# Optimization experiments

Hardware: AMD Instinct MI355X
Metric: run time of the kernel (lower is better)

Reference implementation:

```python
import jax, jax.numpy as jnp
import numpy as np

C, K, D = 64, 512, 2048   # classes, shots per class, hidden_dim
N_ITER = 3                # n_routing_iter


def _squash(x):
    # x: (..., d); squash along last axis: x * ||x|| / (1 + ||x||^2)
    n2 = jnp.sum(x * x, axis=-1, keepdims=True)
    n = jnp.sqrt(n2)
    return x * (n / (1.0 + n2))


def setup_inputs() -> dict:
    key = jax.random.key(0)
    z_s = jax.random.normal(key, (C, K, D), dtype=jnp.float32)
    return {"z_s": z_s}


def reference(z_s):
    # z_s: (C, K, D). All C classes routed in parallel (vectorized over the
    # original Python loop over classes).
    z_sq = _squash(z_s)                       # (C, K, D)
    b = jnp.zeros(z_s.shape[:2], z_s.dtype)   # routing logits (C, K)
    c = jnp.zeros((z_s.shape[0], z_s.shape[2]), z_s.dtype)
    for _ in range(N_ITER):
        d = jax.nn.softmax(b, axis=-1)                      # (C, K)
        c = _squash(jnp.einsum('ck,ckd->cd', d, z_sq))      # (C, D)
        b = b + jnp.einsum('ckd,cd->ck', z_sq, c)           # (C, K)
    # returned representative is c from the LAST iteration (b update after is unused,
    # matching the torch loop where c_i from the final iter is appended)
    return c
```

## Files before the change

### kernel.cpp

```cpp
#include <hip/hip_runtime.h>
#include <math.h>

#define C_CLS   64
#define K_SHOTS 512
#define D_DIM   2048
#define BPC     16
#define ROWS_PER_BLOCK (K_SHOTS / BPC)
#define NWAVES  4
#define ROWS_PER_WAVE (ROWS_PER_BLOCK / NWAVES)
#define NBLK    (C_CLS * BPC)
#define NF4     8

__device__ __forceinline__ float wave_reduce_sum(float v) {
#pragma unroll
    for (int off = 32; off > 0; off >>= 1)
        v += __shfl_xor(v, off, 64);
    return v;
}

template <int PASS>
__global__ __launch_bounds__(256)
void route_pass(const float* __restrict__ z,
                float* __restrict__ scale,
                float* __restrict__ bvec,
                const float* __restrict__ c_prev,
                float* __restrict__ part_s,
                float* __restrict__ part_e)
{
    __shared__ float4 s_comb[NWAVES][D_DIM / 4];
    __shared__ float  e_comb[NWAVES];

    const int rawblk = blockIdx.x;
    const int blk  = (PASS == 1) ? (NBLK - 1 - rawblk) : rawblk;
    const int cls  = blk >> 4;
    const int bic  = blk & (BPC - 1);
    const int lane = threadIdx.x & 63;
    const int wid  = threadIdx.x >> 6;
    const int t    = threadIdx.x;

    float4 cp[NF4];
    if (PASS != 0) {
        const float4* cp4 = (const float4*)(c_prev + (size_t)cls * D_DIM);
#pragma unroll
        for (int i = 0; i < NF4; ++i) cp[i] = cp4[lane + i * 64];
    }

    float4 acc[NF4];
#pragma unroll
    for (int i = 0; i < NF4; ++i) acc[i] = make_float4(0.f, 0.f, 0.f, 0.f);
    float esum = 0.f;

    const int k0 = bic * ROWS_PER_BLOCK + wid * ROWS_PER_WAVE;
    const float4* __restrict__ zbase =
        (const float4*)(z + ((size_t)cls * K_SHOTS + k0) * D_DIM);

    const int r0    = (PASS == 1) ? (ROWS_PER_WAVE - 1) : 0;
    const int rstep = (PASS == 1) ? -1 : 1;

    float4 zcur[NF4];
#pragma unroll
    for (int i = 0; i < NF4; ++i) zcur[i] = zbase[(size_t)r0 * (D_DIM / 4) + lane + i * 64];

#pragma unroll
    for (int rr = 0; rr < ROWS_PER_WAVE; ++rr) {
        const int r = r0 + rr * rstep;
        float4 znext[NF4];
        if (rr + 1 < ROWS_PER_WAVE) {
            const float4* zn = zbase + (size_t)(r + rstep) * (D_DIM / 4);
#pragma unroll
            for (int i = 0; i < NF4; ++i) znext[i] = zn[lane + i * 64];
        }
        const int k = k0 + r;
        float w, sc;
        if (PASS == 0) {
            float n2 = 0.f;
#pragma unroll
            for (int i = 0; i < NF4; ++i)
                n2 += zcur[i].x * zcur[i].x + zcur[i].y * zcur[i].y
                    + zcur[i].z * zcur[i].z + zcur[i].w * zcur[i].w;
            n2 = wave_reduce_sum(n2);
            sc = sqrtf(n2) / (1.f + n2);
            if (lane == 0) scale[cls * K_SHOTS + k] = sc;
            w = 1.f;
        } else {
            float dot = 0.f;
#pragma unroll
            for (int i = 0; i < NF4; ++i)
                dot += zcur[i].x * cp[i].x + zcur[i].y * cp[i].y
                     + zcur[i].z * cp[i].z + zcur[i].w * cp[i].w;
            dot = wave_reduce_sum(dot);
            sc = scale[cls * K_SHOTS + k];
            float bnew = sc * dot;
            if (PASS == 2) bnew += bvec[cls * K_SHOTS + k];
            if (PASS == 1 && lane == 0) bvec[cls * K_SHOTS + k] = bnew;
            w = expf(bnew);
        }
        esum += w;
        const float wsc = w * sc;
#pragma unroll
        for (int i = 0; i < NF4; ++i) {
            acc[i].x += wsc * zcur[i].x;
            acc[i].y += wsc * zcur[i].y;
            acc[i].z += wsc * zcur[i].z;
            acc[i].w += wsc * zcur[i].w;
        }
        if (rr + 1 < ROWS_PER_WAVE) {
#pragma unroll
            for (int i = 0; i < NF4; ++i) zcur[i] = znext[i];
        }
    }

#pragma unroll
    for (int i = 0; i < NF4; ++i) s_comb[wid][lane + i * 64] = acc[i];
    if (lane == 0) e_comb[wid] = esum;
    __syncthreads();

    float4* ps = (float4*)(part_s + (size_t)blk * D_DIM);
#pragma unroll
    for (int j = 0; j < 2; ++j) {
        const int f = t + j * 256;
        const float4 a  = s_comb[0][f];
        const float4 b4 = s_comb[1][f];
        const float4 c4 = s_comb[2][f];
        const float4 d4 = s_comb[3][f];
        float4 s;
        s.x = (a.x + b4.x) + (c4.x + d4.x);
        s.y = (a.y + b4.y) + (c4.y + d4.y);
        s.z = (a.z + b4.z) + (c4.z + d4.z);
        s.w = (a.w + b4.w) + (c4.w + d4.w);
        ps[f] = s;
    }
    if (t == 0) part_e[blk] = (e_comb[0] + e_comb[1]) + (e_comb[2] + e_comb[3]);
}

__global__ __launch_bounds__(256)
void reduce_squash(const float* __restrict__ part_s,
                   const float* __restrict__ part_e,
                   float* __restrict__ c_out)
{
    __shared__ float wred[NWAVES];
    const int cls  = blockIdx.x;
    const int t    = threadIdx.x;
    const int lane = t & 63;
    const int wid  = t >> 6;

    float esum = 0.f;
#pragma unroll
    for (int p = 0; p < BPC; ++p) esum += part_e[cls * BPC + p];
    const float inv = 1.f / esum;

    float4 m[2];
    float n2p = 0.f;
#pragma unroll
    for (int j = 0; j < 2; ++j) {
        const int f = t + j * 256;
        float4 s = make_float4(0.f, 0.f, 0.f, 0.f);
        for (int p = 0; p < BPC; ++p) {
            const float4 v =
                ((const float4*)(part_s + (size_t)(cls * BPC + p) * D_DIM))[f];
            s.x += v.x; s.y += v.y; s.z += v.z; s.w += v.w;
        }
        m[j].x = s.x * inv; m[j].y = s.y * inv;
        m[j].z = s.z * inv; m[j].w = s.w * inv;
        n2p += m[j].x * m[j].x + m[j].y * m[j].y
             + m[j].z * m[j].z + m[j].w * m[j].w;
    }
    float n2 = wave_reduce_sum(n2p);
    if (lane == 0) wred[wid] = n2;
    __syncthreads();
    n2 = (wred[0] + wred[1]) + (wred[2] + wred[3]);
    const float fac = sqrtf(n2) / (1.f + n2);

    float4* co = (float4*)(c_out + (size_t)cls * D_DIM);
#pragma unroll
    for (int j = 0; j < 2; ++j) {
        const int f = t + j * 256;
        float4 o;
        o.x = m[j].x * fac; o.y = m[j].y * fac;
        o.z = m[j].z * fac; o.w = m[j].w * fac;
        co[f] = o;
    }
}

extern "C" void kernel_launch(void* const* d_in, const int* in_sizes, int n_in,
                              void* d_out, int out_size, void* d_ws, size_t ws_size,
                              hipStream_t stream)
{
    const float* z = (const float*)d_in[0];
    float* out = (float*)d_out;
    float* ws  = (float*)d_ws;

    float* scale  = ws;
    float* bvec   = scale + C_CLS * K_SHOTS;
    float* c_buf  = bvec + C_CLS * K_SHOTS;
    float* part_s = c_buf + (size_t)C_CLS * D_DIM;
    float* part_e = part_s + (size_t)NBLK * D_DIM;

    route_pass<0><<<NBLK, 256, 0, stream>>>(z, scale, bvec, nullptr, part_s, part_e);
    reduce_squash<<<C_CLS, 256, 0, stream>>>(part_s, part_e, c_buf);

    route_pass<1><<<NBLK, 256, 0, stream>>>(z, scale, bvec, c_buf, part_s, part_e);
    reduce_squash<<<C_CLS, 256, 0, stream>>>(part_s, part_e, c_buf);

    route_pass<2><<<NBLK, 256, 0, stream>>>(z, scale, bvec, c_buf, part_s, part_e);
    reduce_squash<<<C_CLS, 256, 0, stream>>>(part_s, part_e, out);
}
```

Baseline: 156.6 us.

## Store pre-squashed inputs as fp16 and stream them in later routing passes

The first pass reads fp32 z with nontemporal loads, computes the squash scale, and writes a pre-scaled fp16 copy of z_sq to workspace. The two later routing passes read this half-size copy and drop the per-row scale lookup. This cuts HBM traffic for the bandwidth-bound later passes and may let the fp16 copy stay in the last-level cache. In exchange it adds a 134 MB write, needs a large workspace, and loses precision from fp16 rounding of the inputs.

After: 151.6 us. 1.03x faster.

```diff
diff --git a/kernel.cpp b/kernel.cpp
--- a/kernel.cpp
+++ b/kernel.cpp
@@ -1,4 +1,5 @@
 #include <hip/hip_runtime.h>
+#include <hip/hip_fp16.h>
 #include <math.h>
 
 #define C_CLS   64
@@ -10,6 +11,21 @@
 #define ROWS_PER_WAVE (ROWS_PER_BLOCK / NWAVES)
 #define NBLK    (C_CLS * BPC)
 #define NF4     8
+#define NH4     4
+
+typedef float v4f __attribute__((ext_vector_type(4)));
+
+__device__ __forceinline__ float4 ntload4(const float* p) {
+    v4f v = __builtin_nontemporal_load((const v4f*)p);
+    float4 r; r.x = v.x; r.y = v.y; r.z = v.z; r.w = v.w; return r;
+}
+
+__device__ __forceinline__ uint2 pack4(float4 v) {
+    union { uint2 u; __half2 h[2]; } pk;
+    pk.h[0] = __floats2half2_rn(v.x, v.y);
+    pk.h[1] = __floats2half2_rn(v.z, v.w);
+    return pk.u;
+}
 
 __device__ __forceinline__ float wave_reduce_sum(float v) {
 #pragma unroll
@@ -18,93 +34,62 @@
     return v;
 }
 
-template <int PASS>
 __global__ __launch_bounds__(256)
-void route_pass(const float* __restrict__ z,
-                float* __restrict__ scale,
-                float* __restrict__ bvec,
-                const float* __restrict__ c_prev,
-                float* __restrict__ part_s,
-                float* __restrict__ part_e)
+void route_pass0(const float* __restrict__ z,
+                 __half* __restrict__ z16,
+                 float* __restrict__ part_s,
+                 float* __restrict__ part_e)
 {
     __shared__ float4 s_comb[NWAVES][D_DIM / 4];
     __shared__ float  e_comb[NWAVES];
 
-    const int rawblk = blockIdx.x;
-    const int blk  = (PASS == 1) ? (NBLK - 1 - rawblk) : rawblk;
+    const int blk  = blockIdx.x;
     const int cls  = blk >> 4;
     const int bic  = blk & (BPC - 1);
     const int lane = threadIdx.x & 63;
     const int wid  = threadIdx.x >> 6;
     const int t    = threadIdx.x;
 
-    float4 cp[NF4];
-    if (PASS != 0) {
-        const float4* cp4 = (const float4*)(c_prev + (size_t)cls * D_DIM);
-#pragma unroll
-        for (int i = 0; i < NF4; ++i) cp[i] = cp4[lane + i * 64];
-    }
-
     float4 acc[NF4];
 #pragma unroll
     for (int i = 0; i < NF4; ++i) acc[i] = make_float4(0.f, 0.f, 0.f, 0.f);
     float esum = 0.f;
 
     const int k0 = bic * ROWS_PER_BLOCK + wid * ROWS_PER_WAVE;
-    const float4* __restrict__ zbase =
-        (const float4*)(z + ((size_t)cls * K_SHOTS + k0) * D_DIM);
-
-    const int r0    = (PASS == 1) ? (ROWS_PER_WAVE - 1) : 0;
-    const int rstep = (PASS == 1) ? -1 : 1;
+    const float* __restrict__ zb = z + ((size_t)cls * K_SHOTS + k0) * D_DIM;
 
     float4 zcur[NF4];
 #pragma unroll
-    for (int i = 0; i < NF4; ++i) zcur[i] = zbase[(size_t)r0 * (D_DIM / 4) + lane + i * 64];
-
-#pragma unroll
-    for (int rr = 0; rr < ROWS_PER_WAVE; ++rr) {
-        const int r = r0 + rr * rstep;
+    for (int i = 0; i < NF4; ++i) zcur[i] = ntload4(zb + 4 * (lane + i * 64));
+
+#pragma unroll
+    for (int r = 0; r < ROWS_PER_WAVE; ++r) {
         float4 znext[NF4];
-        if (rr + 1 < ROWS_PER_WAVE) {
-            const float4* zn = zbase + (size_t)(r + rstep) * (D_DIM / 4);
-#pragma unroll
-            for (int i = 0; i < NF4; ++i) znext[i] = zn[lane + i * 64];
-        }
-        const int k = k0 + r;
-        float w, sc;
-        if (PASS == 0) {
-            float n2 = 0.f;
-#pragma unroll
-            for (int i = 0; i < NF4; ++i)
-                n2 += zcur[i].x * zcur[i].x + zcur[i].y * zcur[i].y
-                    + zcur[i].z * zcur[i].z + zcur[i].w * zcur[i].w;
-            n2 = wave_reduce_sum(n2);
-            sc = sqrtf(n2) / (1.f + n2);
-            if (lane == 0) scale[cls * K_SHOTS + k] = sc;
-            w = 1.f;
-        } else {
-            float dot = 0.f;
-#pragma unroll
-            for (int i = 0; i < NF4; ++i)
-                dot += zcur[i].x * cp[i].x + zcur[i].y * cp[i].y
-                     + zcur[i].z * cp[i].z + zcur[i].w * cp[i].w;
-            dot = wave_reduce_sum(dot);
-            sc = scale[cls * K_SHOTS + k];
-            float bnew = sc * dot;
-            if (PASS == 2) bnew += bvec[cls * K_SHOTS + k];
-            if (PASS == 1 && lane == 0) bvec[cls * K_SHOTS + k] = bnew;
-            w = expf(bnew);
-        }
-        esum += w;
-        const float wsc = w * sc;
+        if (r + 1 < ROWS_PER_WAVE) {
+            const float* zn = zb + (size_t)(r + 1) * D_DIM;
+#pragma unroll
+            for (int i = 0; i < NF4; ++i) znext[i] = ntload4(zn + 4 * (lane + i * 64));
+        }
+        float n2 = 0.f;
+#pragma unroll
+        for (int i = 0; i < NF4; ++i)
+            n2 += zcur[i].x * zcur[i].x + zcur[i].y * zcur[i].y
+                + zcur[i].z * zcur[i].z + zcur[i].w * zcur[i].w;
+        n2 = wave_reduce_sum(n2);
+        const float sc = sqrtf(n2) / (1.f + n2);
+
+        uint2* p16 = (uint2*)(z16 + ((size_t)cls * K_SHOTS + k0 + r) * D_DIM);
 #pragma unroll
         for (int i = 0; i < NF4; ++i) {
-            acc[i].x += wsc * zcur[i].x;
-            acc[i].y += wsc * zcur[i].y;
-            acc[i].z += wsc * zcur[i].z;
-            acc[i].w += wsc * zcur[i].w;
-        }
-        if (rr + 1 < ROWS_PER_WAVE) {
+            float4 s;
+            s.x = sc * zcur[i].x; s.y = sc * zcur[i].y;
+            s.z = sc * zcur[i].z; s.w = sc * zcur[i].w;
+            p16[lane + i * 64] = pack4(s);
+            acc[i].x += s.x; acc[i].y += s.y; acc[i].z += s.z; acc[i].w += s.w;
+        }
+        esum += 1.f;
+
+        if (r + 1 < ROWS_PER_WAVE) {
 #pragma unroll
             for (int i = 0; i < NF4; ++i) zcur[i] = znext[i];
         }
@@ -133,6 +118,129 @@
     if (t == 0) part_e[blk] = (e_comb[0] + e_comb[1]) + (e_comb[2] + e_comb[3]);
 }
 
+template <int PASS>
+__global__ __launch_bounds__(256)
+void route_pass_h(const __half* __restrict__ z16,
+                  float* __restrict__ bvec,
+                  const float* __restrict__ c_prev,
+                  float* __restrict__ part_s,
+                  float* __restrict__ part_e)
+{
+    __shared__ float4 s_comb[NWAVES][D_DIM / 4];
+    __shared__ float  e_comb[NWAVES];
+
+    const int rawblk = blockIdx.x;
+    const int blk  = (PASS == 1) ? (NBLK - 1 - rawblk) : rawblk;
+    const int cls  = blk >> 4;
+    const int bic  = blk & (BPC - 1);
+    const int lane = threadIdx.x & 63;
+    const int wid  = threadIdx.x >> 6;
+    const int t    = threadIdx.x;
+
+    const float4* cp4 = (const float4*)(c_prev + (size_t)cls * D_DIM);
+    float4 cpA[NH4], cpB[NH4];
+#pragma unroll
+    for (int j = 0; j < NH4; ++j) {
+        const int c2i = 2 * (lane + j * 64);
+        cpA[j] = cp4[c2i];
+        cpB[j] = cp4[c2i + 1];
+    }
+
+    float4 acc[2 * NH4];
+#pragma unroll
+    for (int i = 0; i < 2 * NH4; ++i) acc[i] = make_float4(0.f, 0.f, 0.f, 0.f);
+    float esum = 0.f;
+
+    const int k0 = bic * ROWS_PER_BLOCK + wid * ROWS_PER_WAVE;
+    const float4* __restrict__ zb =
+        (const float4*)(z16 + ((size_t)cls * K_SHOTS + k0) * D_DIM);
+
+    const int r0    = (PASS == 1) ? (ROWS_PER_WAVE - 1) : 0;
+    const int rstep = (PASS == 1) ? -1 : 1;
+
+    float4 zcur[NH4];
+#pragma unroll
+    for (int j = 0; j < NH4; ++j)
+        zcur[j] = zb[(size_t)r0 * (D_DIM / 8) + lane + j * 64];
+
+#pragma unroll
+    for (int rr = 0; rr < ROWS_PER_WAVE; ++rr) {
+        const int r = r0 + rr * rstep;
+        float4 znext[NH4];
+        if (rr + 1 < ROWS_PER_WAVE) {
+            const float4* zn = zb + (size_t)(r + rstep) * (D_DIM / 8);
+#pragma unroll
+            for (int j = 0; j < NH4; ++j) znext[j] = zn[lane + j * 64];
+        }
+
+        float dot = 0.f;
+#pragma unroll
+        for (int j = 0; j < NH4; ++j) {
+            const __half2* hp = (const __half2*)&zcur[j];
+            const float2 a0 = __half22float2(hp[0]);
+            const float2 a1 = __half22float2(hp[1]);
+            const float2 a2 = __half22float2(hp[2]);
+            const float2 a3 = __half22float2(hp[3]);
+            dot += a0.x * cpA[j].x + a0.y * cpA[j].y
+                 + a1.x * cpA[j].z + a1.y * cpA[j].w
+                 + a2.x * cpB[j].x + a2.y * cpB[j].y
+                 + a3.x * cpB[j].z + a3.y * cpB[j].w;
+        }
+        dot = wave_reduce_sum(dot);
+
+        const int k = k0 + r;
+        float bnew = dot;
+        if (PASS == 2) bnew += bvec[cls * K_SHOTS + k];
+        if (PASS == 1 && lane == 0) bvec[cls * K_SHOTS + k] = bnew;
+        const float w = expf(bnew);
+        esum += w;
+
+#pragma unroll
+        for (int j = 0; j < NH4; ++j) {
+            const __half2* hp = (const __half2*)&zcur[j];
+            const float2 a0 = __half22float2(hp[0]);
+            const float2 a1 = __half22float2(hp[1]);
+            const float2 a2 = __half22float2(hp[2]);
+            const float2 a3 = __half22float2(hp[3]);
+            acc[2 * j].x     += w * a0.x;  acc[2 * j].y     += w * a0.y;
+            acc[2 * j].z     += w * a1.x;  acc[2 * j].w     += w * a1.y;
+            acc[2 * j + 1].x += w * a2.x;  acc[2 * j + 1].y += w * a2.y;
+            acc[2 * j + 1].z += w * a3.x;  acc[2 * j + 1].w += w * a3.y;
+        }
+
+        if (rr + 1 < ROWS_PER_WAVE) {
+#pragma unroll
+            for (int j = 0; j < NH4; ++j) zcur[j] = znext[j];
+        }
+    }
+
+#pragma unroll
+    for (int j = 0; j < NH4; ++j) {
+        const int c2i = 2 * (lane + j * 64);
+        s_comb[wid][c2i]     = acc[2 * j];
+        s_comb[wid][c2i + 1] = acc[2 * j + 1];
+    }
+    if (lane == 0) e_comb[wid] = esum;
+    __syncthreads();
+
+    float4* ps = (float4*)(part_s + (size_t)blk * D_DIM);
+#pragma unroll
+    for (int j = 0; j < 2; ++j) {
+        const int f = t + j * 256;
+        const float4 a  = s_comb[0][f];
+        const float4 b4 = s_comb[1][f];
+        const float4 c4 = s_comb[2][f];
+        const float4 d4 = s_comb[3][f];
+        float4 s;
+        s.x = (a.x + b4.x) + (c4.x + d4.x);
+        s.y = (a.y + b4.y) + (c4.y + d4.y);
+        s.z = (a.z + b4.z) + (c4.z + d4.z);
+        s.w = (a.w + b4.w) + (c4.w + d4.w);
+        ps[f] = s;
+    }
+    if (t == 0) part_e[blk] = (e_comb[0] + e_comb[1]) + (e_comb[2] + e_comb[3]);
+}
+
 __global__ __launch_bounds__(256)
 void reduce_squash(const float* __restrict__ part_s,
                    const float* __restrict__ part_e,
@@ -190,18 +298,18 @@
     float* out = (float*)d_out;
     float* ws  = (float*)d_ws;
 
-    float* scale  = ws;
-    float* bvec   = scale + C_CLS * K_SHOTS;
+    float* bvec   = ws;
     float* c_buf  = bvec + C_CLS * K_SHOTS;
     float* part_s = c_buf + (size_t)C_CLS * D_DIM;
     float* part_e = part_s + (size_t)NBLK * D_DIM;
-
-    route_pass<0><<<NBLK, 256, 0, stream>>>(z, scale, bvec, nullptr, part_s, part_e);
+    __half* z16   = (__half*)(part_e + NBLK);
+
+    route_pass0<<<NBLK, 256, 0, stream>>>(z, z16, part_s, part_e);
     reduce_squash<<<C_CLS, 256, 0, stream>>>(part_s, part_e, c_buf);
 
-    route_pass<1><<<NBLK, 256, 0, stream>>>(z, scale, bvec, c_buf, part_s, part_e);
+    route_pass_h<1><<<NBLK, 256, 0, stream>>>(z16, bvec, c_buf, part_s, part_e);
     reduce_squash<<<C_CLS, 256, 0, stream>>>(part_s, part_e, c_buf);
 
-    route_pass<2><<<NBLK, 256, 0, stream>>>(z, scale, bvec, c_buf, part_s, part_e);
+    route_pass_h<2><<<NBLK, 256, 0, stream>>>(z16, bvec, c_buf, part_s, part_e);
     reduce_squash<<<C_CLS, 256, 0, stream>>>(part_s, part_e, out);
 }
```
